# Kernel optimization log

Hardware: AMD Instinct MI355X
Metric: run time of the kernel (lower is better)

## Reference

```python
import jax, jax.numpy as jnp
import numpy as np


def _pad_kernel_like(kernel_oc0, H, W, ks):
    # torch: F.pad(k,(p,p,p,p)) then if shape mismatch F.pad(k,(0,1,0,1))
    p = (H - ks) // 2
    extra = H - (ks + 2 * p)  # 0 or 1
    return jnp.pad(kernel_oc0, ((0, 0), (p, p + extra), (p, p + extra)))


def setup_inputs() -> dict:
    key = jax.random.key(0)
    k1, k2 = jax.random.split(key)
    B, C, H, W = 8, 16, 128, 128
    O, KS = 32, 9
    x = jax.random.normal(k1, (B, C, H, W), dtype=jnp.float32)
    # kaiming_uniform-ish init scale
    fan_in = C * KS * KS
    bound = float(np.sqrt(6.0 / fan_in))
    kernel = jax.random.uniform(k2, (O, C, KS, KS), dtype=jnp.float32,
                                minval=-bound, maxval=bound)
    return {"x": x, "kernel": kernel}


def reference(x, kernel):
    # x: [B,C,H,W] float32, kernel: [O,C,ks,ks] float32
    B, C, H, W = x.shape
    O, ks = kernel.shape[0], kernel.shape[-1]
    # Faithful to original bug: only kernel[:, 0] is used for every input channel.
    k = _pad_kernel_like(kernel[:, 0], H, W, ks)  # [O,H,W]
    # 4f optical FFT convolution: ifftshift -> FFT -> multiply -> IFFT -> fftshift -> |.|
    Fx = jnp.fft.fft2(jnp.fft.ifftshift(x, axes=(-2, -1)))   # [B,C,H,W] complex64
    Fk = jnp.fft.fft2(jnp.fft.ifftshift(k, axes=(-2, -1)))   # [O,H,W]   complex64
    prod = Fx[:, None, :, :, :] * Fk[None, :, None, :, :]    # [B,O,C,H,W]
    field = jnp.fft.fftshift(jnp.fft.ifft2(prod), axes=(-2, -1))
    out_pc = jnp.abs(field)                                  # per-(out,in)-channel intensity
    return out_pc.sum(axis=2)                                # [B,O,H,W]
```

## Files before the change

### kernel.cpp

```cpp
#include <hip/hip_runtime.h>


typedef __attribute__((ext_vector_type(8)))  short  short8;
typedef __attribute__((ext_vector_type(4)))  float  float4v;
typedef __attribute__((ext_vector_type(4)))  unsigned int uint4v;

#define XR_ROWS 138
#define XR_RDW  72
#define XR_CH_DW (XR_ROWS * XR_RDW)
#define XR_TOT_DW (128 * XR_CH_DW)
#define BPRE_OFF ((size_t)128 * XR_ROWS * 288)
#define CHB 3168
#define PREP_BLOCKS 2048
#define PREP_STRIDE (PREP_BLOCKS * 256)

__device__ __forceinline__ unsigned int f2bf(float f) {
    union { float f; unsigned int u; } a; a.f = f;
    unsigned int u = a.u;
    u += 0x7fffu + ((u >> 16) & 1u);
    return u >> 16;
}

#if __has_builtin(__builtin_amdgcn_alignbit)
#define ALIGN16(hi_, lo_) __builtin_amdgcn_alignbit((hi_), (lo_), 16)
#else
#define ALIGN16(hi_, lo_) \
    (unsigned int)((((unsigned long long)(hi_) << 32) | (lo_)) >> 16)
#endif

#define FRAG_EVEN(q_) __builtin_bit_cast(short8, (uint4v){                    \
        wnd[(q_)+0], wnd[(q_)+1], wnd[(q_)+2], wnd[(q_)+3]})
#define FRAG_ODD(q_)  __builtin_bit_cast(short8, (uint4v){                    \
        ALIGN16(wnd[(q_)+1], wnd[(q_)+0]),                                    \
        ALIGN16(wnd[(q_)+2], wnd[(q_)+1]),                                    \
        ALIGN16(wnd[(q_)+3], wnd[(q_)+2]),                                    \
        ALIGN16(wnd[(q_)+4], wnd[(q_)+3])})

__device__ __forceinline__ void gload_lds16(const void* g, void* l) {
    __builtin_amdgcn_global_load_lds(
        (const __attribute__((address_space(1))) unsigned int*)g,
        (__attribute__((address_space(3))) unsigned int*)l, 16, 0, 0);
}

__global__ __launch_bounds__(256)
void optical_prep_69698729279498(const float* __restrict__ x,
                                 const float* __restrict__ kern,
                                 unsigned int* __restrict__ xr,
                                 uint4v* __restrict__ bpre) {
    if (blockIdx.x == PREP_BLOCKS) {
        const int l = threadIdx.x;
        if (l < 64) {
            const int lk = l & 15;
            const int g2 = l >> 4;
            for (int oh = 0; oh < 2; ++oh) {
                const int o = oh * 16 + lk;
                for (int ck = 0; ck < 5; ++ck) {
                    const int ti  = 2 * ck + (g2 >> 1);
                    const int tj0 = (g2 & 1) * 8;
                    unsigned int pk[4];
#pragma unroll
                    for (int ee = 0; ee < 4; ++ee) {
                        int tj_a = tj0 + 2 * ee, tj_b = tj_a + 1;
                        float va = (ti <= 8 && tj_a <= 8) ? kern[o * 1296 + ti * 9 + tj_a] : 0.f;
                        float vb = (ti <= 8 && tj_b <= 8) ? kern[o * 1296 + ti * 9 + tj_b] : 0.f;
                        pk[ee] = f2bf(va) | (f2bf(vb) << 16);
                    }
                    bpre[(oh * 5 + ck) * 64 + l] = (uint4v){pk[0], pk[1], pk[2], pk[3]};
                }
            }
        }
        return;
    }
    for (int idx = blockIdx.x * 256 + threadIdx.x; idx < XR_TOT_DW;
         idx += PREP_STRIDE) {
        int bc  = idx / XR_CH_DW;
        int rem = idx - bc * XR_CH_DW;
        int r   = rem / XR_RDW;
        int ccd = rem - r * XR_RDW;
        int cc  = 2 * ccd;
        const float* xp = x + (bc << 14) + ((r & 127) << 7);
        float v0 = xp[(132 - cc) & 127];
        float v1 = xp[(131 - cc) & 127];
        xr[idx] = f2bf(v0) | (f2bf(v1) << 16);
    }
}

__global__ __launch_bounds__(256, 2)
void optical_conv_69698729279498(const unsigned int* __restrict__ xr,
                                 const uint4v* __restrict__ bpre,
                                 float* __restrict__ out) {
    __shared__ __align__(16) unsigned short ldsb[16 * (CHB / 2)];

    const int tid = threadIdx.x;
    const int l   = tid & 63;
    const int w   = tid >> 6;
    const int oh  = w & 1;
    const int rh  = w >> 1;
    const int i0  = blockIdx.x * 2;
    const int b   = blockIdx.y;

    const int lk   = l & 15;
    const int g    = (l >> 4) & 1;
    const int hi32 = l >> 5;
    const int g2   = l >> 4;
    const int o    = oh * 16 + lk;

    const int wstart = (i0 >= 4) ? (i0 - 4) : (i0 + 124);
    const char* xr8 = (const char*)xr;
#pragma unroll
    for (int cw = 0; cw < 4; ++cw) {
        const int ch = 4 * w + cw;
        const char* src = xr8 + ((size_t)((b * 16 + ch) * XR_ROWS + wstart)) * 288;
        char* dst = (char*)ldsb + ch * CHB;
        gload_lds16(src + 0 * 1024 + l * 16, dst + 0 * 1024);
        gload_lds16(src + 1 * 1024 + l * 16, dst + 1 * 1024);
        gload_lds16(src + 2 * 1024 + l * 16, dst + 2 * 1024);
        if (l < 6)
            gload_lds16(src + 3072 + l * 16, dst + 3072);
    }

    short8 Bf[5];
#pragma unroll
    for (int ck = 0; ck < 5; ++ck)
        Bf[ck] = __builtin_bit_cast(short8, bpre[(oh * 5 + ck) * 64 + l]);

    __syncthreads();

    float4v acc[8];
#pragma unroll
    for (int p = 0; p < 8; ++p) acc[p] = (float4v){0.f, 0.f, 0.f, 0.f};
    const float4v zero4 = (float4v){0.f, 0.f, 0.f, 0.f};

    const char* lb = (const char*)ldsb
                   + (240 - 16 * lk + 16 * g) + (1 - hi32 + rh) * 288;

    for (int c = 0; c < 16; ++c) {
        uint4v wa[5], wb[5];
#pragma unroll
        for (int ck = 0; ck < 5; ++ck) {
            const char* p = lb + (8 - 2 * ck) * 288;
            wa[ck] = *(const uint4v*)p;
            wb[ck] = *(const uint4v*)(p + 16);
        }
        float4v D[8];
#pragma unroll
        for (int ck = 0; ck < 5; ++ck) {
            unsigned int wnd[8] = {wa[ck].x, wa[ck].y, wa[ck].z, wa[ck].w,
                                   wb[ck].x, wb[ck].y, wb[ck].z, wb[ck].w};
            short8 f0 = FRAG_ODD(3),  f1 = FRAG_EVEN(3);
            short8 f2 = FRAG_ODD(2),  f3 = FRAG_EVEN(2);
            short8 f4 = FRAG_ODD(1),  f5 = FRAG_EVEN(1);
            short8 f6 = FRAG_ODD(0),  f7 = FRAG_EVEN(0);
            D[0] = __builtin_amdgcn_mfma_f32_16x16x32_bf16(f0, Bf[ck], ck ? D[0] : zero4, 0, 0, 0);
            D[1] = __builtin_amdgcn_mfma_f32_16x16x32_bf16(f1, Bf[ck], ck ? D[1] : zero4, 0, 0, 0);
            D[2] = __builtin_amdgcn_mfma_f32_16x16x32_bf16(f2, Bf[ck], ck ? D[2] : zero4, 0, 0, 0);
            D[3] = __builtin_amdgcn_mfma_f32_16x16x32_bf16(f3, Bf[ck], ck ? D[3] : zero4, 0, 0, 0);
            D[4] = __builtin_amdgcn_mfma_f32_16x16x32_bf16(f4, Bf[ck], ck ? D[4] : zero4, 0, 0, 0);
            D[5] = __builtin_amdgcn_mfma_f32_16x16x32_bf16(f5, Bf[ck], ck ? D[5] : zero4, 0, 0, 0);
            D[6] = __builtin_amdgcn_mfma_f32_16x16x32_bf16(f6, Bf[ck], ck ? D[6] : zero4, 0, 0, 0);
            D[7] = __builtin_amdgcn_mfma_f32_16x16x32_bf16(f7, Bf[ck], ck ? D[7] : zero4, 0, 0, 0);
        }
#pragma unroll
        for (int p = 0; p < 8; ++p)
#pragma unroll
            for (int e = 0; e < 4; ++e) acc[p][e] += fabsf(D[p][e]);
        lb += CHB;
    }

    const int i = i0 + rh;
    float* ob = out + ((((size_t)(b * 32 + o)) * 128 + i) << 7);
#pragma unroll
    for (int e = 0; e < 4; ++e) {
        float4v lo = (float4v){acc[0][e], acc[1][e], acc[2][e], acc[3][e]};
        float4v hi = (float4v){acc[4][e], acc[5][e], acc[6][e], acc[7][e]};
        *(float4v*)&ob[32 * g2 + 8 * e]     = lo;
        *(float4v*)&ob[32 * g2 + 8 * e + 4] = hi;
    }
}

extern "C" void kernel_launch(void* const* d_in, const int* in_sizes, int n_in,
                              void* d_out, int out_size, void* d_ws, size_t ws_size,
                              hipStream_t stream) {
    const float* x = (const float*)d_in[0];
    const float* kern = (const float*)d_in[1];
    float* out = (float*)d_out;
    unsigned int* xr = (unsigned int*)d_ws;
    uint4v* bpre = (uint4v*)((char*)d_ws + BPRE_OFF);

    hipLaunchKernelGGL(optical_prep_69698729279498, dim3(PREP_BLOCKS + 1),
                       dim3(256), 0, stream, x, kern, xr, bpre);
    hipLaunchKernelGGL(optical_conv_69698729279498, dim3(64, 8), dim3(256),
                       0, stream, xr, bpre, out);
}
```

Before: 94.75 us.

## Split channel loop across two wave groups with LDS reduction

Doubles the conv block to 512 threads, with each half of the waves handling 8 of the 16 input channels, then reduces partial sums through LDS before the store. Per-channel loads are now interleaved with the MFMA loop instead of prefetched for all five taps. The goal is more waves in flight to hide LDS latency and shorten the per-wave serial chain, at the cost of an extra barrier, LDS round trip for the reduction, and higher register pressure under the launch bound of 4.

```diff
diff --git a/kernel.cpp b/kernel.cpp
--- a/kernel.cpp
+++ b/kernel.cpp
@@ -85,7 +85,7 @@
     }
 }
 
-__global__ __launch_bounds__(256, 2)
+__global__ __launch_bounds__(512, 4)
 void optical_conv_69698729279498(const unsigned int* __restrict__ xr,
                                  const uint4v* __restrict__ bpre,
                                  float* __restrict__ out) {
@@ -95,7 +95,8 @@
     const int l   = tid & 63;
     const int w   = tid >> 6;
     const int oh  = w & 1;
-    const int rh  = w >> 1;
+    const int rh  = (w >> 1) & 1;
+    const int cg  = w >> 2;
     const int i0  = blockIdx.x * 2;
     const int b   = blockIdx.y;
 
@@ -108,8 +109,8 @@
     const int wstart = (i0 >= 4) ? (i0 - 4) : (i0 + 124);
     const char* xr8 = (const char*)xr;
 #pragma unroll
-    for (int cw = 0; cw < 4; ++cw) {
-        const int ch = 4 * w + cw;
+    for (int cw = 0; cw < 2; ++cw) {
+        const int ch = 2 * w + cw;
         const char* src = xr8 + ((size_t)((b * 16 + ch) * XR_ROWS + wstart)) * 288;
         char* dst = (char*)ldsb + ch * CHB;
         gload_lds16(src + 0 * 1024 + l * 16, dst + 0 * 1024);
@@ -132,21 +133,18 @@
     const float4v zero4 = (float4v){0.f, 0.f, 0.f, 0.f};
 
     const char* lb = (const char*)ldsb
-                   + (240 - 16 * lk + 16 * g) + (1 - hi32 + rh) * 288;
-
-    for (int c = 0; c < 16; ++c) {
-        uint4v wa[5], wb[5];
+                   + (240 - 16 * lk + 16 * g) + (1 - hi32 + rh) * 288
+                   + cg * 8 * CHB;
+
+    for (int c = 0; c < 8; ++c) {
+        float4v D[8];
 #pragma unroll
         for (int ck = 0; ck < 5; ++ck) {
             const char* p = lb + (8 - 2 * ck) * 288;
-            wa[ck] = *(const uint4v*)p;
-            wb[ck] = *(const uint4v*)(p + 16);
-        }
-        float4v D[8];
-#pragma unroll
-        for (int ck = 0; ck < 5; ++ck) {
-            unsigned int wnd[8] = {wa[ck].x, wa[ck].y, wa[ck].z, wa[ck].w,
-                                   wb[ck].x, wb[ck].y, wb[ck].z, wb[ck].w};
+            uint4v w0 = *(const uint4v*)p;
+            uint4v w1 = *(const uint4v*)(p + 16);
+            unsigned int wnd[8] = {w0.x, w0.y, w0.z, w0.w,
+                                   w1.x, w1.y, w1.z, w1.w};
             short8 f0 = FRAG_ODD(3),  f1 = FRAG_EVEN(3);
             short8 f2 = FRAG_ODD(2),  f3 = FRAG_EVEN(2);
             short8 f4 = FRAG_ODD(1),  f5 = FRAG_EVEN(1);
@@ -167,14 +165,31 @@
         lb += CHB;
     }
 
-    const int i = i0 + rh;
-    float* ob = out + ((((size_t)(b * 32 + o)) * 128 + i) << 7);
-#pragma unroll
-    for (int e = 0; e < 4; ++e) {
-        float4v lo = (float4v){acc[0][e], acc[1][e], acc[2][e], acc[3][e]};
-        float4v hi = (float4v){acc[4][e], acc[5][e], acc[6][e], acc[7][e]};
-        *(float4v*)&ob[32 * g2 + 8 * e]     = lo;
-        *(float4v*)&ob[32 * g2 + 8 * e + 4] = hi;
+    __syncthreads();
+    float* red = (float*)ldsb;
+    const int rbase = ((w & 3) * 64 + l) * 36;
+    if (cg == 1) {
+#pragma unroll
+        for (int p = 0; p < 8; ++p)
+            *(float4v*)&red[rbase + 4 * p] = acc[p];
+    }
+    __syncthreads();
+    if (cg == 0) {
+#pragma unroll
+        for (int p = 0; p < 8; ++p) {
+            float4v r = *(const float4v*)&red[rbase + 4 * p];
+#pragma unroll
+            for (int e = 0; e < 4; ++e) acc[p][e] += r[e];
+        }
+        const int i = i0 + rh;
+        float* ob = out + ((((size_t)(b * 32 + o)) * 128 + i) << 7);
+#pragma unroll
+        for (int e = 0; e < 4; ++e) {
+            float4v lo = (float4v){acc[0][e], acc[1][e], acc[2][e], acc[3][e]};
+            float4v hi = (float4v){acc[4][e], acc[5][e], acc[6][e], acc[7][e]};
+            *(float4v*)&ob[32 * g2 + 8 * e]     = lo;
+            *(float4v*)&ob[32 * g2 + 8 * e + 4] = hi;
+        }
     }
 }
 
@@ -189,6 +204,6 @@
 
     hipLaunchKernelGGL(optical_prep_69698729279498, dim3(PREP_BLOCKS + 1),
                        dim3(256), 0, stream, x, kern, xr, bpre);
-    hipLaunchKernelGGL(optical_conv_69698729279498, dim3(64, 8), dim3(256),
+    hipLaunchKernelGGL(optical_conv_69698729279498, dim3(64, 8), dim3(512),
                        0, stream, xr, bpre, out);
 }
```

After: 95.31 us. No clear change (+0.6%).

## Replace LDS staging with direct global loads and register double-buffering

Applied to the files above, without the earlier changes.

The conv kernel no longer stages each block's 16-channel input windows into shared memory with global_load_lds followed by a barrier. Each lane now reads its overlapping window straight from the global workspace into registers, and the next channel's window is prefetched while the MFMAs for the current channel run. This removes the LDS footprint and the block-wide sync, which may allow more blocks per CU and hide load latency. In exchange, overlapping lanes issue redundant global/L1 loads, and the extra prefetch registers raise VGPR pressure.

```diff
diff --git a/kernel.cpp b/kernel.cpp
--- a/kernel.cpp
+++ b/kernel.cpp
@@ -8,9 +8,9 @@
 #define XR_ROWS 138
 #define XR_RDW  72
 #define XR_CH_DW (XR_ROWS * XR_RDW)
+#define XR_CH_B  (XR_CH_DW * 4)
 #define XR_TOT_DW (128 * XR_CH_DW)
 #define BPRE_OFF ((size_t)128 * XR_ROWS * 288)
-#define CHB 3168
 #define PREP_BLOCKS 2048
 #define PREP_STRIDE (PREP_BLOCKS * 256)
 
@@ -35,12 +35,6 @@
         ALIGN16(wnd[(q_)+2], wnd[(q_)+1]),                                    \
         ALIGN16(wnd[(q_)+3], wnd[(q_)+2]),                                    \
         ALIGN16(wnd[(q_)+4], wnd[(q_)+3])})
-
-__device__ __forceinline__ void gload_lds16(const void* g, void* l) {
-    __builtin_amdgcn_global_load_lds(
-        (const __attribute__((address_space(1))) unsigned int*)g,
-        (__attribute__((address_space(3))) unsigned int*)l, 16, 0, 0);
-}
 
 __global__ __launch_bounds__(256)
 void optical_prep_69698729279498(const float* __restrict__ x,
@@ -85,12 +79,23 @@
     }
 }
 
+struct Win { uint4v a[5]; uint4v b[5]; };
+
+__device__ __forceinline__ Win loadwin(const char* p) {
+    Win W;
+#pragma unroll
+    for (int ck = 0; ck < 5; ++ck) {
+        const char* q = p + (8 - 2 * ck) * 288;
+        W.a[ck] = *(const uint4v*)q;
+        W.b[ck] = *(const uint4v*)(q + 16);
+    }
+    return W;
+}
+
 __global__ __launch_bounds__(256, 2)
 void optical_conv_69698729279498(const unsigned int* __restrict__ xr,
                                  const uint4v* __restrict__ bpre,
                                  float* __restrict__ out) {
-    __shared__ __align__(16) unsigned short ldsb[16 * (CHB / 2)];
-
     const int tid = threadIdx.x;
     const int l   = tid & 63;
     const int w   = tid >> 6;
@@ -106,47 +111,31 @@
     const int o    = oh * 16 + lk;
 
     const int wstart = (i0 >= 4) ? (i0 - 4) : (i0 + 124);
-    const char* xr8 = (const char*)xr;
-#pragma unroll
-    for (int cw = 0; cw < 4; ++cw) {
-        const int ch = 4 * w + cw;
-        const char* src = xr8 + ((size_t)((b * 16 + ch) * XR_ROWS + wstart)) * 288;
-        char* dst = (char*)ldsb + ch * CHB;
-        gload_lds16(src + 0 * 1024 + l * 16, dst + 0 * 1024);
-        gload_lds16(src + 1 * 1024 + l * 16, dst + 1 * 1024);
-        gload_lds16(src + 2 * 1024 + l * 16, dst + 2 * 1024);
-        if (l < 6)
-            gload_lds16(src + 3072 + l * 16, dst + 3072);
-    }
+    const char* base = (const char*)xr
+                     + (size_t)(b * 16) * XR_CH_B
+                     + (size_t)(wstart + 1 - hi32 + rh) * 288
+                     + (240 - 16 * lk + 16 * g);
 
     short8 Bf[5];
 #pragma unroll
     for (int ck = 0; ck < 5; ++ck)
         Bf[ck] = __builtin_bit_cast(short8, bpre[(oh * 5 + ck) * 64 + l]);
 
-    __syncthreads();
-
     float4v acc[8];
 #pragma unroll
     for (int p = 0; p < 8; ++p) acc[p] = (float4v){0.f, 0.f, 0.f, 0.f};
     const float4v zero4 = (float4v){0.f, 0.f, 0.f, 0.f};
 
-    const char* lb = (const char*)ldsb
-                   + (240 - 16 * lk + 16 * g) + (1 - hi32 + rh) * 288;
+    Win cur = loadwin(base);
+    for (int c = 0; c < 16; ++c) {
+        const int cn = (c < 15) ? (c + 1) : 15;
+        Win nxt = loadwin(base + (size_t)cn * XR_CH_B);
 
-    for (int c = 0; c < 16; ++c) {
-        uint4v wa[5], wb[5];
-#pragma unroll
-        for (int ck = 0; ck < 5; ++ck) {
-            const char* p = lb + (8 - 2 * ck) * 288;
-            wa[ck] = *(const uint4v*)p;
-            wb[ck] = *(const uint4v*)(p + 16);
-        }
         float4v D[8];
 #pragma unroll
         for (int ck = 0; ck < 5; ++ck) {
-            unsigned int wnd[8] = {wa[ck].x, wa[ck].y, wa[ck].z, wa[ck].w,
-                                   wb[ck].x, wb[ck].y, wb[ck].z, wb[ck].w};
+            unsigned int wnd[8] = {cur.a[ck].x, cur.a[ck].y, cur.a[ck].z, cur.a[ck].w,
+                                   cur.b[ck].x, cur.b[ck].y, cur.b[ck].z, cur.b[ck].w};
             short8 f0 = FRAG_ODD(3),  f1 = FRAG_EVEN(3);
             short8 f2 = FRAG_ODD(2),  f3 = FRAG_EVEN(2);
             short8 f4 = FRAG_ODD(1),  f5 = FRAG_EVEN(1);
@@ -164,7 +153,8 @@
         for (int p = 0; p < 8; ++p)
 #pragma unroll
             for (int e = 0; e < 4; ++e) acc[p][e] += fabsf(D[p][e]);
-        lb += CHB;
+
+        cur = nxt;
     }
 
     const int i = i0 + rh;
```

Result: slower. 102.9 us (+8.6%).
